# Performance work log

Measured on AMD Instinct MI355X. Metric: run time of the kernel, lower is better.

Reference implementation:

```python
import jax, jax.numpy as jnp
import numpy as np

E, D, H, K = 640000, 128, 64, 8  # edges, edge-feat dim, hidden=max(32, D//2), n_experts
TEMPERATURE = 1.0


def setup_inputs() -> dict:
    key = jax.random.key(0)
    ks = jax.random.split(key, 6)
    u = lambda k, shape, fan: jax.random.uniform(k, shape, jnp.float32, -1.0 / np.sqrt(fan), 1.0 / np.sqrt(fan))
    return {
        "edge_features": jax.random.normal(ks[0], (E, D), jnp.float32),
        "w1": u(ks[1], (D, H), D),
        "b1": u(ks[2], (H,), D),
        "w2": u(ks[3], (H, K), H),
        "b2": u(ks[4], (K,), H),
        "w_proj": u(ks[5], (D, K), D),
    }


def reference(edge_features, w1, b1, w2, b2, w_proj):
    # edge MLP router: [E, D] -> [E, H] -> [E, K]
    h = jax.nn.relu(edge_features @ w1 + b1)
    logits = (h @ w2 + b2) / TEMPERATURE
    # soft gating
    alpha = jax.nn.softmax(logits, axis=-1)  # [E, K]
    # expert scores (no bias) and weighted reduce
    expert_scores = edge_features @ w_proj   # [E, K]
    fused_edge = jnp.sum(alpha * expert_scores, axis=-1)  # [E]
    return fused_edge, alpha
```

## Files before the change

kernel.cpp:

```cpp
#include <hip/hip_runtime.h>
#include <hip/hip_bf16.h>

typedef __bf16 bf16x8 __attribute__((ext_vector_type(8)));
typedef float  f32x4  __attribute__((ext_vector_type(4)));

#define MFMA(a, b, c) __builtin_amdgcn_mfma_f32_16x16x32_bf16((a), (b), (c), 0, 0, 0)


__device__ __forceinline__ int swz(int row, int byteInRow) {
    return row * 256 + (byteInRow ^ ((row & 7) << 4));
}

__global__ __launch_bounds__(256, 4) void edge_moe_kernel(
    const float* __restrict__ x,  const float* __restrict__ w1,
    const float* __restrict__ b1, const float* __restrict__ w2,
    const float* __restrict__ b2, const float* __restrict__ wp,
    float* __restrict__ outFused, float* __restrict__ outAlpha, int E)
{
    __shared__ __align__(16) char lds[32768];
    char* XH = lds;
    char* HF = lds + 16384;

    const int tid  = threadIdx.x;
    const int lane = tid & 63;
    const int wid  = tid >> 6;
    const int lc   = lane & 15;
    const int lg   = lane >> 4;

    bf16x8 w1h[4];
#pragma unroll
    for (int kk = 0; kk < 4; ++kk) {
        bf16x8 h;
#pragma unroll
        for (int j = 0; j < 8; ++j) {
            int kidx = kk * 32 + lg * 8 + j;
            h[j] = (__bf16)w1[kidx * 64 + wid * 16 + lc];
        }
        w1h[kk] = h;
    }
    bf16x8 w2h[2], w2l[2];
#pragma unroll
    for (int kk = 0; kk < 2; ++kk) {
        bf16x8 h, l;
#pragma unroll
        for (int j = 0; j < 8; ++j) {
            int kidx = kk * 32 + lg * 8 + j;
            float v = (lc < 8) ? w2[kidx * 8 + lc] : 0.0f;
            __bf16 hb = (__bf16)v;
            h[j] = hb; l[j] = (__bf16)(v - (float)hb);
        }
        w2h[kk] = h; w2l[kk] = l;
    }
    bf16x8 wph[4];
#pragma unroll
    for (int kk = 0; kk < 4; ++kk) {
        bf16x8 h;
#pragma unroll
        for (int j = 0; j < 8; ++j) {
            int kidx = kk * 32 + lg * 8 + j;
            h[j] = (lc < 8) ? (__bf16)wp[kidx * 8 + lc] : (__bf16)0.0f;
        }
        wph[kk] = h;
    }
    const float b1v = b1[wid * 16 + lc];
    const float b2v = (lc < 8) ? b2[lc] : 0.0f;

    const int ntiles = (E + 63) >> 6;
    const int r0 = tid >> 4;
    const int c8 = tid & 15;
    const int arow = wid * 16 + lc;

    for (int tile = blockIdx.x; tile < ntiles; tile += gridDim.x) {
        const long long eb = (long long)tile * 64;

        float4 vr[4][2];
#pragma unroll
        for (int it = 0; it < 4; ++it) {
            long long e = eb + r0 + it * 16;
            if (e > (long long)E - 1) e = E - 1;
            const float4* p = (const float4*)(x + (size_t)e * 128 + c8 * 8);
            vr[it][0] = p[0];
            vr[it][1] = p[1];
        }
        __syncthreads();

#pragma unroll
        for (int it = 0; it < 4; ++it) {
            int row = r0 + it * 16;
            bf16x8 h;
            const float* f = (const float*)&vr[it][0];
#pragma unroll
            for (int j = 0; j < 8; ++j) h[j] = (__bf16)f[j];
            *(bf16x8*)(XH + swz(row, c8 * 16)) = h;
        }
        __syncthreads();

        bf16x8 axh[4];
        f32x4 acc[4] = {{0.f,0.f,0.f,0.f},{0.f,0.f,0.f,0.f},{0.f,0.f,0.f,0.f},{0.f,0.f,0.f,0.f}};
#pragma unroll
        for (int kk = 0; kk < 4; ++kk) {
            axh[kk] = *(const bf16x8*)(XH + swz(arow, kk * 64 + lg * 16));
            acc[0] = MFMA(axh[kk], w1h[kk], acc[0]);
        }
#pragma unroll
        for (int mtt = 1; mtt < 4; ++mtt) {
            const int mt = (wid + mtt) & 3;
            const int row = mt * 16 + lc;
#pragma unroll
            for (int kk = 0; kk < 4; ++kk) {
                bf16x8 ah = *(const bf16x8*)(XH + swz(row, kk * 64 + lg * 16));
                acc[mtt] = MFMA(ah, w1h[kk], acc[mtt]);
            }
        }
#pragma unroll
        for (int mtt = 0; mtt < 4; ++mtt) {
            const int mt = (wid + mtt) & 3;
#pragma unroll
            for (int r = 0; r < 4; ++r) {
                float hv = fmaxf(acc[mtt][r] + b1v, 0.f);
                *(float*)(HF + swz(mt * 16 + lg * 4 + r, (wid * 16 + lc) * 4)) = hv;
            }
        }
        __syncthreads();

        f32x4 lac = {0.f, 0.f, 0.f, 0.f};
        f32x4 sac = {0.f, 0.f, 0.f, 0.f};
#pragma unroll
        for (int kk = 0; kk < 2; ++kk) {
            int base = kk * 128 + lg * 32;
            f32x4 h0 = *(const f32x4*)(HF + swz(arow, base));
            f32x4 h1 = *(const f32x4*)(HF + swz(arow, base + 16));
            bf16x8 hh;
#pragma unroll
            for (int j = 0; j < 4; ++j) {
                hh[j]     = (__bf16)h0[j];
                hh[j + 4] = (__bf16)h1[j];
            }
            lac = MFMA(hh, w2h[kk], lac);
            lac = MFMA(hh, w2l[kk], lac);
        }
#pragma unroll
        for (int kk = 0; kk < 4; ++kk) {
            sac = MFMA(axh[kk], wph[kk], sac);
        }

#pragma unroll
        for (int r = 0; r < 4; ++r) {
            float lv = lac[r] + b2v;
            float p = __expf(lv);
            float s  = p;
            float fs = p * sac[r];
            s  += __shfl_xor(s, 1);  fs += __shfl_xor(fs, 1);
            s  += __shfl_xor(s, 2);  fs += __shfl_xor(fs, 2);
            s  += __shfl_xor(s, 4);  fs += __shfl_xor(fs, 4);
            float inv = 1.0f / s;
            float alpha = p * inv;
            float fv = fs * inv;
            long long edge = eb + wid * 16 + lg * 4 + r;
            if (edge < E) {
                if (lc < 8) outAlpha[edge * 8 + lc] = alpha;
                if (lc == 0) outFused[edge] = fv;
            }
        }
    }
}

extern "C" void kernel_launch(void* const* d_in, const int* in_sizes, int n_in,
                              void* d_out, int out_size, void* d_ws, size_t ws_size,
                              hipStream_t stream) {
    const float* x  = (const float*)d_in[0];
    const float* w1 = (const float*)d_in[1];
    const float* b1 = (const float*)d_in[2];
    const float* w2 = (const float*)d_in[3];
    const float* b2 = (const float*)d_in[4];
    const float* wp = (const float*)d_in[5];

    const int E = in_sizes[0] / 128;
    float* outF = (float*)d_out;
    float* outA = outF + E;

    const int ntiles = (E + 63) >> 6;
    const int blocks = ntiles < 1024 ? ntiles : 1024;
    edge_moe_kernel<<<blocks, 256, 0, stream>>>(x, w1, b1, w2, b2, wp, outF, outA, E);
}
```

Measured before the change: 77.66 us.

## Make waves independent: per-wave X rows from global, W1 fragments in LDS

Each wave now loads its own 16 edge rows straight from global memory into MFMA A-fragments, and computes all 64 hidden columns for them, with W1 fragments staged once in LDS. The hidden activations go through a private per-wave LDS region, so the per-tile __syncthreads barriers are gone. The cost is more LDS reads of W1 per tile and less coalesced 32-byte-per-lane global loads. Occupancy bound is lowered to 3 blocks per CU to allow more registers. Without a barrier, correctness of the per-wave LDS round trip relies on wave-level lockstep and compiler memory fences.

```diff
diff --git a/kernel.cpp b/kernel.cpp
--- a/kernel.cpp
+++ b/kernel.cpp
@@ -11,33 +11,36 @@
     return row * 256 + (byteInRow ^ ((row & 7) << 4));
 }
 
-__global__ __launch_bounds__(256, 4) void edge_moe_kernel(
+__global__ __launch_bounds__(256, 3) void edge_moe_kernel(
     const float* __restrict__ x,  const float* __restrict__ w1,
     const float* __restrict__ b1, const float* __restrict__ w2,
     const float* __restrict__ b2, const float* __restrict__ wp,
     float* __restrict__ outFused, float* __restrict__ outAlpha, int E)
 {
     __shared__ __align__(16) char lds[32768];
-    char* XH = lds;
-    char* HF = lds + 16384;
+    char* W1F = lds;
+    char* HFB = lds + 16384;
 
     const int tid  = threadIdx.x;
     const int lane = tid & 63;
     const int wid  = tid >> 6;
     const int lc   = lane & 15;
     const int lg   = lane >> 4;
+    char* HFW = HFB + wid * 4096;
 
-    bf16x8 w1h[4];
 #pragma unroll
-    for (int kk = 0; kk < 4; ++kk) {
+    for (int i = 0; i < 4; ++i) {
+        int combo = wid * 4 + i;
+        int kk = combo >> 2, nt = combo & 3;
         bf16x8 h;
 #pragma unroll
         for (int j = 0; j < 8; ++j) {
             int kidx = kk * 32 + lg * 8 + j;
-            h[j] = (__bf16)w1[kidx * 64 + wid * 16 + lc];
+            h[j] = (__bf16)w1[kidx * 64 + nt * 16 + lc];
         }
-        w1h[kk] = h;
+        *(bf16x8*)(W1F + combo * 1024 + lane * 16) = h;
     }
+
     bf16x8 w2h[2], w2l[2];
 #pragma unroll
     for (int kk = 0; kk < 2; ++kk) {
@@ -62,74 +65,62 @@
         }
         wph[kk] = h;
     }
-    const float b1v = b1[wid * 16 + lc];
+    float b1v[4];
+#pragma unroll
+    for (int nt = 0; nt < 4; ++nt) b1v[nt] = b1[nt * 16 + lc];
     const float b2v = (lc < 8) ? b2[lc] : 0.0f;
 
+    __syncthreads();
+
     const int ntiles = (E + 63) >> 6;
-    const int r0 = tid >> 4;
-    const int c8 = tid & 15;
-    const int arow = wid * 16 + lc;
 
     for (int tile = blockIdx.x; tile < ntiles; tile += gridDim.x) {
         const long long eb = (long long)tile * 64;
 
-        float4 vr[4][2];
+        long long e = eb + wid * 16 + lc;
+        if (e > (long long)E - 1) e = (long long)E - 1;
+        const float* xr = x + (size_t)e * 128;
+
+        bf16x8 axh[4];
 #pragma unroll
-        for (int it = 0; it < 4; ++it) {
-            long long e = eb + r0 + it * 16;
-            if (e > (long long)E - 1) e = E - 1;
-            const float4* p = (const float4*)(x + (size_t)e * 128 + c8 * 8);
-            vr[it][0] = p[0];
-            vr[it][1] = p[1];
+        for (int kk = 0; kk < 4; ++kk) {
+            const f32x4* p = (const f32x4*)(xr + kk * 32 + lg * 8);
+            f32x4 x0 = p[0];
+            f32x4 x1 = p[1];
+            bf16x8 a;
+#pragma unroll
+            for (int j = 0; j < 4; ++j) {
+                a[j]     = (__bf16)x0[j];
+                a[j + 4] = (__bf16)x1[j];
+            }
+            axh[kk] = a;
         }
-        __syncthreads();
+
+        f32x4 acc[4] = {{0.f,0.f,0.f,0.f},{0.f,0.f,0.f,0.f},{0.f,0.f,0.f,0.f},{0.f,0.f,0.f,0.f}};
+#pragma unroll
+        for (int kk = 0; kk < 4; ++kk)
+#pragma unroll
+            for (int nt = 0; nt < 4; ++nt) {
+                bf16x8 wf = *(const bf16x8*)(W1F + (kk * 4 + nt) * 1024 + lane * 16);
+                acc[nt] = MFMA(axh[kk], wf, acc[nt]);
+            }
 
 #pragma unroll
-        for (int it = 0; it < 4; ++it) {
-            int row = r0 + it * 16;
-            bf16x8 h;
-            const float* f = (const float*)&vr[it][0];
-#pragma unroll
-            for (int j = 0; j < 8; ++j) h[j] = (__bf16)f[j];
-            *(bf16x8*)(XH + swz(row, c8 * 16)) = h;
-        }
-        __syncthreads();
-
-        bf16x8 axh[4];
-        f32x4 acc[4] = {{0.f,0.f,0.f,0.f},{0.f,0.f,0.f,0.f},{0.f,0.f,0.f,0.f},{0.f,0.f,0.f,0.f}};
-#pragma unroll
-        for (int kk = 0; kk < 4; ++kk) {
-            axh[kk] = *(const bf16x8*)(XH + swz(arow, kk * 64 + lg * 16));
-            acc[0] = MFMA(axh[kk], w1h[kk], acc[0]);
-        }
-#pragma unroll
-        for (int mtt = 1; mtt < 4; ++mtt) {
-            const int mt = (wid + mtt) & 3;
-            const int row = mt * 16 + lc;
-#pragma unroll
-            for (int kk = 0; kk < 4; ++kk) {
-                bf16x8 ah = *(const bf16x8*)(XH + swz(row, kk * 64 + lg * 16));
-                acc[mtt] = MFMA(ah, w1h[kk], acc[mtt]);
-            }
-        }
-#pragma unroll
-        for (int mtt = 0; mtt < 4; ++mtt) {
-            const int mt = (wid + mtt) & 3;
+        for (int nt = 0; nt < 4; ++nt)
 #pragma unroll
             for (int r = 0; r < 4; ++r) {
-                float hv = fmaxf(acc[mtt][r] + b1v, 0.f);
-                *(float*)(HF + swz(mt * 16 + lg * 4 + r, (wid * 16 + lc) * 4)) = hv;
+                float hv = fmaxf(acc[nt][r] + b1v[nt], 0.f);
+                *(float*)(HFW + swz(lg * 4 + r, (nt * 16 + lc) * 4)) = hv;
             }
-        }
-        __syncthreads();
+        asm volatile("" ::: "memory");
 
         f32x4 lac = {0.f, 0.f, 0.f, 0.f};
         f32x4 sac = {0.f, 0.f, 0.f, 0.f};
 #pragma unroll
         for (int kk = 0; kk < 2; ++kk) {
             int base = kk * 128 + lg * 32;
-            f32x4 h0 = *(const f32x4*)(HF + swz(arow, base));
-            f32x4 h1 = *(const f32x4*)(HF + swz(arow, base + 16));
+            f32x4 h0 = *(const f32x4*)(HFW + swz(lc, base));
+            f32x4 h1 = *(const f32x4*)(HFW + swz(lc, base + 16));
             bf16x8 hh;
 #pragma unroll
             for (int j = 0; j < 4; ++j) {
@@ -143,6 +134,7 @@
         for (int kk = 0; kk < 4; ++kk) {
             sac = MFMA(axh[kk], wph[kk], sac);
         }
+        asm volatile("" ::: "memory");
 
 #pragma unroll
         for (int r = 0; r < 4; ++r) {
```

Measured after the change: 77.68 us. Within noise of the previous version (+0.0%).
